# Kernel optimization log

Hardware: AMD Instinct MI355X
Metric: run time of the kernel (lower is better)

Reference implementation:

```python
import jax, jax.numpy as jnp
import numpy as np

KK = 27  # 3x3x3 kernel taps


def conv3d(x, w, b):
    # plain 3D conv, stride 1, pad 1 (the offset-prediction conv)
    y = jax.lax.conv_general_dilated(
        x, w, window_strides=(1, 1, 1),
        padding=((1, 1), (1, 1), (1, 1)),
        dimension_numbers=('NCDHW', 'OIDHW', 'NCDHW'))
    return y + b[None, :, None, None, None]


def deform_conv3d_hw(x, offset, weight):
    # DCN with 3x3x3 kernel, offsets only along H,W (dimension='HW');
    # temporal tap positions are integers so trilinear -> bilinear in HW.
    N, C, T, H, W = x.shape
    off = offset.reshape(N, KK, 2, T, H, W)  # interleaved (h_off, w_off) per tap
    kk = jnp.arange(KK)
    kt = kk // 9 - 1
    kh = (kk // 3) % 3 - 1
    kw = kk % 3 - 1
    t_idx = jnp.arange(T)[None, :, None, None] + kt[:, None, None, None]  # (KK,T,1,1)
    t_ok = jnp.broadcast_to((t_idx >= 0) & (t_idx < T), (KK, T, H, W))
    t_cb = jnp.broadcast_to(jnp.clip(t_idx, 0, T - 1), (KK, T, H, W))
    ph = (jnp.arange(H)[None, None, :, None] + kh[:, None, None, None]).astype(x.dtype)[None] + off[:, :, 0]
    pw = (jnp.arange(W)[None, None, None, :] + kw[:, None, None, None]).astype(x.dtype)[None] + off[:, :, 1]
    h0f = jnp.floor(ph); w0f = jnp.floor(pw)
    lh = (ph - h0f)[:, None]  # (N,1,KK,T,H,W)
    lw = (pw - w0f)[:, None]
    h0 = h0f.astype(jnp.int32); w0 = w0f.astype(jnp.int32)
    h1 = h0 + 1; w1 = w0 + 1

    def gather(hi, wi):
        ok = t_ok[None] & (hi >= 0) & (hi < H) & (wi >= 0) & (wi < W)
        hic = jnp.clip(hi, 0, H - 1)
        wic = jnp.clip(wi, 0, W - 1)
        def g1(xb, okb, hb, wb):
            # xb: (C,T,H,W); index arrays: (KK,T,H,W) -> (C,KK,T,H,W)
            return jnp.where(okb[None], xb[:, t_cb, hb, wb], 0.0)
        return jax.vmap(g1)(x, ok, hic, wic)  # (N,C,KK,T,H,W)

    acc = gather(h0, w0) * ((1 - lh) * (1 - lw))
    acc = acc + gather(h0, w1) * ((1 - lh) * lw)
    acc = acc + gather(h1, w0) * (lh * (1 - lw))
    acc = acc + gather(h1, w1) * (lh * lw)
    Cout = weight.shape[0]
    return jnp.einsum('nckthw,ock->nothw', acc, weight.reshape(Cout, C, KK))


def setup_inputs() -> dict:
    key = jax.random.key(0)
    ks = jax.random.split(key, 7)
    N, C, T, H, W = 1, 64, 7, 64, 64
    x = jax.random.normal(ks[0], (N, C, T, H, W), jnp.float32)
    sc_off = 0.01  # keep predicted offsets small (original zero-inits them)
    sc_w = 1.0 / np.sqrt(C * KK)
    w_off0 = jax.random.normal(ks[1], (2 * KK, C, 3, 3, 3), jnp.float32) * sc_off
    b_off0 = jax.random.normal(ks[2], (2 * KK,), jnp.float32) * sc_off
    w0 = jax.random.normal(ks[3], (C, C, 3, 3, 3), jnp.float32) * sc_w
    w_off1 = jax.random.normal(ks[4], (2 * KK, C, 3, 3, 3), jnp.float32) * sc_off
    b_off1 = jax.random.normal(ks[5], (2 * KK,), jnp.float32) * sc_off
    w1 = jax.random.normal(ks[6], (C, C, 3, 3, 3), jnp.float32) * sc_w
    return {"x": x, "w_off0": w_off0, "b_off0": b_off0, "w0": w0,
            "w_off1": w_off1, "b_off1": b_off1, "w1": w1}


def reference(x, w_off0, b_off0, w0, w_off1, b_off1, w1):
    y = deform_conv3d_hw(x, conv3d(x, w_off0, b_off0), w0)
    y = jax.nn.leaky_relu(y, negative_slope=0.1)
    y = deform_conv3d_hw(y, conv3d(y, w_off1, b_off1), w1)
    return y + x
```

## Files before the change

### kernel.cpp

```cpp
#include <hip/hip_runtime.h>

#define T_ 7
#define H_ 64
#define W_ 64
#define KK_ 27
#define HW_ 4096
#define THW_ 28672
#define CO_OFF 54
#define OFFSTR 56

using frag_ab = __attribute__((ext_vector_type(8))) short;
using f32x4   = __attribute__((ext_vector_type(4))) float;

__device__ __forceinline__ unsigned short f2bf(float v) {
    unsigned u = __float_as_uint(v);
    unsigned r = u + 0x7FFFu + ((u >> 16) & 1u);
    return (unsigned short)(r >> 16);
}
__device__ __forceinline__ float bf2f(unsigned short h) {
    return __uint_as_float(((unsigned)h) << 16);
}
__device__ __forceinline__ void split_bf(float v, unsigned short& hi, unsigned short& lo) {
    hi = f2bf(v);
    lo = f2bf(v - bf2f(hi));
}
__device__ __forceinline__ void split_tr(float v, unsigned short& hi, unsigned short& lo) {
    unsigned u = __float_as_uint(v);
    hi = (unsigned short)(u >> 16);
    float r = v - __uint_as_float(u & 0xFFFF0000u);
    lo = (unsigned short)(__float_as_uint(r) >> 16);
}

__global__ void prep_wt_kernel(const float* __restrict__ w_off0,
                               const float* __restrict__ w_off1,
                               const float* __restrict__ w0,
                               const float* __restrict__ w1,
                               unsigned short* __restrict__ wc0,
                               unsigned short* __restrict__ wc1,
                               unsigned short* __restrict__ wd0,
                               unsigned short* __restrict__ wd1) {
    int idx = blockIdx.x * 256 + threadIdx.x;
    int which = idx / 110592;
    int r = idx - which * 110592;
    int tap = r >> 12;
    int o = (r >> 6) & 63;
    int c = r & 63;
    const float* src;
    unsigned short* dst;
    int Co;
    switch (which) {
        case 0:  src = w_off0; dst = wc0; Co = CO_OFF; break;
        case 1:  src = w_off1; dst = wc1; Co = CO_OFF; break;
        case 2:  src = w0;     dst = wd0; Co = 64;     break;
        default: src = w1;     dst = wd1; Co = 64;     break;
    }
    float v = 0.f;
    if (o < Co) v = src[o * 1728 + c * 27 + tap];
    unsigned short hi, lo;
    split_bf(v, hi, lo);
    dst[tap * 8192 + 0 * 4096 + o * 64 + c] = hi;
    dst[tap * 8192 + 1 * 4096 + o * 64 + c] = lo;
}

__global__ void __launch_bounds__(256) transpose_kernel(
    const float* __restrict__ x, float* __restrict__ xT) {
    __shared__ float lx[64][65];
    const int tid = threadIdx.x;
    const int base = blockIdx.x * 64;
    const int w = tid & 63, cg = tid >> 6;
#pragma unroll
    for (int i = 0; i < 16; ++i) {
        const int c = cg * 16 + i;
        lx[c][w] = x[c * THW_ + base + w];
    }
    __syncthreads();
    const int c = tid & 63, j0 = tid >> 6;
#pragma unroll
    for (int j = 0; j < 16; ++j) {
        const int wp = j * 4 + j0;
        xT[(base + wp) * 64 + c] = lx[c][wp];
    }
}


__global__ void __launch_bounds__(512, 8) conv_off_kernel(
    const float* __restrict__ xT, const unsigned short* __restrict__ wB,
    const float* __restrict__ bias, float* __restrict__ offT) {
    __shared__ __align__(16) unsigned short A_l[2][32][64];
    __shared__ __align__(16) unsigned short B_l[2][64][64];
    const int tid = threadIdx.x;
    const int bid = blockIdx.x;
    const int t = bid >> 7, h = (bid >> 1) & 63, wh = bid & 1;
    const int wg = wh * 32;
    const int c4 = tid & 15;
    const int wp = tid >> 4;
    const int lane = tid & 63, wid = tid >> 6;
    const int wtile = wid & 1, otile = wid >> 1;
    const int ln15 = lane & 15, kg = lane >> 4;
    const int arow = wtile * 16 + ln15;
    const int brow = otile * 16 + ln15;
    const int posb = t * HW_ + h * W_ + wg;
    const int bo = (tid >> 3) & 63, bc8 = tid & 7;
    const int bi = (bc8 * 8) ^ ((bo & 7) << 3);

    f32x4 acc = {0.f, 0.f, 0.f, 0.f};

    for (int k = 0; k < KK_; ++k) {
        const int kt = k / 9 - 1, kh = (k / 3) % 3 - 1, kw = k % 3 - 1;
        const int ts = t + kt, hs = h + kh, wsr = wg + wp + kw;
        const bool ok = ((unsigned)ts < 7u) & ((unsigned)hs < 64u) & ((unsigned)wsr < 64u);
        float4 v = make_float4(0.f, 0.f, 0.f, 0.f);
        if (ok)
            v = *reinterpret_cast<const float4*>(xT + (ts * HW_ + hs * W_ + wsr) * 64 + c4 * 4);
        ushort4 hv, lv;
        split_tr(v.x, hv.x, lv.x); split_tr(v.y, hv.y, lv.y);
        split_tr(v.z, hv.z, lv.z); split_tr(v.w, hv.w, lv.w);
        const int ci = (c4 * 4) ^ ((wp & 7) << 3);
        *reinterpret_cast<ushort4*>(&A_l[0][wp][ci]) = hv;
        *reinterpret_cast<ushort4*>(&A_l[1][wp][ci]) = lv;
        const unsigned short* wt = wB + k * 8192 + bo * 64 + bc8 * 8;
        *reinterpret_cast<frag_ab*>(&B_l[0][bo][bi]) =
            *reinterpret_cast<const frag_ab*>(wt);
        *reinterpret_cast<frag_ab*>(&B_l[1][bo][bi]) =
            *reinterpret_cast<const frag_ab*>(wt + 4096);
        __syncthreads();
#pragma unroll
        for (int ks = 0; ks < 2; ++ks) {
            const int ka = ks * 32 + kg * 8;
            const frag_ab ah = *reinterpret_cast<const frag_ab*>(&A_l[0][arow][ka ^ ((arow & 7) << 3)]);
            const frag_ab al = *reinterpret_cast<const frag_ab*>(&A_l[1][arow][ka ^ ((arow & 7) << 3)]);
            const frag_ab bh = *reinterpret_cast<const frag_ab*>(&B_l[0][brow][ka ^ ((brow & 7) << 3)]);
            const frag_ab bl = *reinterpret_cast<const frag_ab*>(&B_l[1][brow][ka ^ ((brow & 7) << 3)]);
            acc = __builtin_amdgcn_mfma_f32_16x16x32_bf16(ah, bh, acc, 0, 0, 0);
            acc = __builtin_amdgcn_mfma_f32_16x16x32_bf16(ah, bl, acc, 0, 0, 0);
            acc = __builtin_amdgcn_mfma_f32_16x16x32_bf16(al, bh, acc, 0, 0, 0);
        }
        __syncthreads();
    }

    const int o = otile * 16 + ln15;
    if (o < CO_OFF) {
        const float b = bias[o];
#pragma unroll
        for (int reg = 0; reg < 4; ++reg) {
            const int wl_ = wtile * 16 + kg * 4 + reg;
            offT[(posb + wl_) * OFFSTR + o] = acc[reg] + b;
        }
    }
}

template <int MODE>
__global__ void __launch_bounds__(512, 8) dcn_kernel(
    const float* __restrict__ xT, const float* __restrict__ offT,
    const unsigned short* __restrict__ wB, const float* __restrict__ resid,
    float* __restrict__ out) {
    __shared__ __align__(16) unsigned short A_l[2][32][64];
    __shared__ __align__(16) unsigned short B_l[2][64][64];
    __shared__ float ep[32][65];
    const int tid = threadIdx.x;
    const int bid = blockIdx.x;
    const int t = bid >> 7, h = (bid >> 1) & 63, wh = bid & 1;
    const int wg = wh * 32;
    const int c4 = tid & 15;
    const int wp = tid >> 4;
    const int lane = tid & 63, wid = tid >> 6;
    const int wtile = wid & 1, otile = wid >> 1;
    const int ln15 = lane & 15, kg = lane >> 4;
    const int arow = wtile * 16 + ln15;
    const int brow = otile * 16 + ln15;
    const int posb = t * HW_ + h * W_ + wg;
    const int bo = (tid >> 3) & 63, bc8 = tid & 7;
    const int bi = (bc8 * 8) ^ ((bo & 7) << 3);

    f32x4 acc = {0.f, 0.f, 0.f, 0.f};
    const int w = wg + wp;
    const float* offp = offT + (posb + wp) * OFFSTR;

    for (int k = 0; k < KK_; ++k) {
        const int kt = k / 9 - 1, kh = (k / 3) % 3 - 1, kw = k % 3 - 1;
        const int ts = t + kt;
        const bool tok = (unsigned)ts < 7u;
        const int tcb = ts < 0 ? 0 : (ts > 6 ? 6 : ts);
        const float2 of2 = *reinterpret_cast<const float2*>(offp + 2 * k);
        const float ph = (float)(h + kh) + of2.x;
        const float pw = (float)(w + kw) + of2.y;
        const float h0f = floorf(ph), w0f = floorf(pw);
        const float fh = ph - h0f, fw = pw - w0f;
        const int h0 = (int)h0f, w0i = (int)w0f;
        const int h1 = h0 + 1, w1i = w0i + 1;
        const bool h0k = (unsigned)h0 < 64u, h1k = (unsigned)h1 < 64u;
        const bool w0k = (unsigned)w0i < 64u, w1k = (unsigned)w1i < 64u;
        const int tb = tcb * HW_;
        const int h0c = (h0 < 0 ? 0 : (h0 > 63 ? 63 : h0)) * W_;
        const int h1c = (h1 < 0 ? 0 : (h1 > 63 ? 63 : h1)) * W_;
        const int w0c = w0i < 0 ? 0 : (w0i > 63 ? 63 : w0i);
        const int w1c = w1i < 0 ? 0 : (w1i > 63 ? 63 : w1i);
        const float f0 = (tok && h0k && w0k) ? (1.f - fh) * (1.f - fw) : 0.f;
        const float f1 = (tok && h0k && w1k) ? (1.f - fh) * fw : 0.f;
        const float f2 = (tok && h1k && w0k) ? fh * (1.f - fw) : 0.f;
        const float f3 = (tok && h1k && w1k) ? fh * fw : 0.f;
        const int cb = c4 * 4;
        const float4 A = *reinterpret_cast<const float4*>(xT + (tb + h0c + w0c) * 64 + cb);
        const float4 B = *reinterpret_cast<const float4*>(xT + (tb + h0c + w1c) * 64 + cb);
        const float4 C = *reinterpret_cast<const float4*>(xT + (tb + h1c + w0c) * 64 + cb);
        const float4 D = *reinterpret_cast<const float4*>(xT + (tb + h1c + w1c) * 64 + cb);
        float s0 = fmaf(f0, A.x, fmaf(f1, B.x, fmaf(f2, C.x, f3 * D.x)));
        float s1 = fmaf(f0, A.y, fmaf(f1, B.y, fmaf(f2, C.y, f3 * D.y)));
        float s2 = fmaf(f0, A.z, fmaf(f1, B.z, fmaf(f2, C.z, f3 * D.z)));
        float s3 = fmaf(f0, A.w, fmaf(f1, B.w, fmaf(f2, C.w, f3 * D.w)));
        ushort4 hv, lv;
        split_tr(s0, hv.x, lv.x); split_tr(s1, hv.y, lv.y);
        split_tr(s2, hv.z, lv.z); split_tr(s3, hv.w, lv.w);
        const int ci = (cb) ^ ((wp & 7) << 3);
        *reinterpret_cast<ushort4*>(&A_l[0][wp][ci]) = hv;
        *reinterpret_cast<ushort4*>(&A_l[1][wp][ci]) = lv;
        const unsigned short* wt = wB + k * 8192 + bo * 64 + bc8 * 8;
        *reinterpret_cast<frag_ab*>(&B_l[0][bo][bi]) =
            *reinterpret_cast<const frag_ab*>(wt);
        *reinterpret_cast<frag_ab*>(&B_l[1][bo][bi]) =
            *reinterpret_cast<const frag_ab*>(wt + 4096);
        __syncthreads();
#pragma unroll
        for (int ks = 0; ks < 2; ++ks) {
            const int ka = ks * 32 + kg * 8;
            const frag_ab ah = *reinterpret_cast<const frag_ab*>(&A_l[0][arow][ka ^ ((arow & 7) << 3)]);
            const frag_ab al = *reinterpret_cast<const frag_ab*>(&A_l[1][arow][ka ^ ((arow & 7) << 3)]);
            const frag_ab bh = *reinterpret_cast<const frag_ab*>(&B_l[0][brow][ka ^ ((brow & 7) << 3)]);
            const frag_ab bl = *reinterpret_cast<const frag_ab*>(&B_l[1][brow][ka ^ ((brow & 7) << 3)]);
            acc = __builtin_amdgcn_mfma_f32_16x16x32_bf16(ah, bh, acc, 0, 0, 0);
            acc = __builtin_amdgcn_mfma_f32_16x16x32_bf16(ah, bl, acc, 0, 0, 0);
            acc = __builtin_amdgcn_mfma_f32_16x16x32_bf16(al, bh, acc, 0, 0, 0);
        }
        __syncthreads();
    }

    const int o = otile * 16 + ln15;
    if (MODE == 0) {
#pragma unroll
        for (int reg = 0; reg < 4; ++reg) {
            const int wl_ = wtile * 16 + kg * 4 + reg;
            float v = acc[reg];
            v = v > 0.f ? v : 0.1f * v;
            out[(posb + wl_) * 64 + o] = v;
        }
    } else {
#pragma unroll
        for (int reg = 0; reg < 4; ++reg) {
            const int wl_ = wtile * 16 + kg * 4 + reg;
            ep[wl_][o] = acc[reg];
        }
        __syncthreads();
        const int w2 = tid & 31, og = tid >> 5;
#pragma unroll
        for (int i = 0; i < 4; ++i) {
            const int oc = og + i * 16;
            out[oc * THW_ + posb + w2] = ep[w2][oc] + resid[oc * THW_ + posb + w2];
        }
    }
}

extern "C" void kernel_launch(void* const* d_in, const int* in_sizes, int n_in,
                              void* d_out, int out_size, void* d_ws, size_t ws_size,
                              hipStream_t stream) {
    (void)in_sizes; (void)n_in; (void)out_size; (void)ws_size;
    const float* x      = (const float*)d_in[0];
    const float* w_off0 = (const float*)d_in[1];
    const float* b_off0 = (const float*)d_in[2];
    const float* w0     = (const float*)d_in[3];
    const float* w_off1 = (const float*)d_in[4];
    const float* b_off1 = (const float*)d_in[5];
    const float* w1     = (const float*)d_in[6];
    float* out = (float*)d_out;

    float* ws = (float*)d_ws;
    float* xT   = ws;
    float* yT   = xT + 64 * THW_;
    float* offT = yT + 64 * THW_;
    unsigned short* wc0 = (unsigned short*)(offT + THW_ * OFFSTR);
    unsigned short* wc1 = wc0 + 221184;
    unsigned short* wd0 = wc1 + 221184;
    unsigned short* wd1 = wd0 + 221184;

    prep_wt_kernel<<<1728, 256, 0, stream>>>(w_off0, w_off1, w0, w1,
                                             wc0, wc1, wd0, wd1);
    transpose_kernel<<<448, 256, 0, stream>>>(x, xT);
    conv_off_kernel<<<896, 512, 0, stream>>>(xT, wc0, b_off0, offT);
    dcn_kernel<0><<<896, 512, 0, stream>>>(xT, offT, wd0, nullptr, yT);
    conv_off_kernel<<<896, 512, 0, stream>>>(yT, wc1, b_off1, offT);
    dcn_kernel<1><<<896, 512, 0, stream>>>(yT, offT, wd1, x, out);
}
```

Baseline: 265.4 us.

## Prefetch next tap's inputs and weights into registers during MFMA

Both the offset conv kernel and the deformable conv kernel now issue the global loads for the next kernel tap (input samples, bilinear corners, offsets, weights) into registers before running the current tap's MFMAs. The results are written to shared memory after a barrier, so global memory latency is meant to overlap with matrix compute. The cost is higher register pressure, which could reduce occupancy under launch_bounds(512,8). Each iteration also now has two barriers.

```diff
diff --git a/kernel.cpp b/kernel.cpp
--- a/kernel.cpp
+++ b/kernel.cpp
@@ -102,12 +102,12 @@
     const int posb = t * HW_ + h * W_ + wg;
     const int bo = (tid >> 3) & 63, bc8 = tid & 7;
     const int bi = (bc8 * 8) ^ ((bo & 7) << 3);
+    const int ci = (c4 * 4) ^ ((wp & 7) << 3);
 
     f32x4 acc = {0.f, 0.f, 0.f, 0.f};
 
-    for (int k = 0; k < KK_; ++k) {
-        const int kt = k / 9 - 1, kh = (k / 3) % 3 - 1, kw = k % 3 - 1;
-        const int ts = t + kt, hs = h + kh, wsr = wg + wp + kw;
+    {
+        const int ts = t - 1, hs = h - 1, wsr = wg + wp - 1;
         const bool ok = ((unsigned)ts < 7u) & ((unsigned)hs < 64u) & ((unsigned)wsr < 64u);
         float4 v = make_float4(0.f, 0.f, 0.f, 0.f);
         if (ok)
@@ -115,15 +115,29 @@
         ushort4 hv, lv;
         split_tr(v.x, hv.x, lv.x); split_tr(v.y, hv.y, lv.y);
         split_tr(v.z, hv.z, lv.z); split_tr(v.w, hv.w, lv.w);
-        const int ci = (c4 * 4) ^ ((wp & 7) << 3);
         *reinterpret_cast<ushort4*>(&A_l[0][wp][ci]) = hv;
         *reinterpret_cast<ushort4*>(&A_l[1][wp][ci]) = lv;
-        const unsigned short* wt = wB + k * 8192 + bo * 64 + bc8 * 8;
-        *reinterpret_cast<frag_ab*>(&B_l[0][bo][bi]) =
-            *reinterpret_cast<const frag_ab*>(wt);
-        *reinterpret_cast<frag_ab*>(&B_l[1][bo][bi]) =
-            *reinterpret_cast<const frag_ab*>(wt + 4096);
-        __syncthreads();
+        const unsigned short* wt = wB + bo * 64 + bc8 * 8;
+        *reinterpret_cast<frag_ab*>(&B_l[0][bo][bi]) = *reinterpret_cast<const frag_ab*>(wt);
+        *reinterpret_cast<frag_ab*>(&B_l[1][bo][bi]) = *reinterpret_cast<const frag_ab*>(wt + 4096);
+    }
+    __syncthreads();
+
+    float4 vn;
+    frag_ab b0n, b1n;
+    for (int k = 0; k < KK_; ++k) {
+        if (k + 1 < KK_) {
+            const int kk = k + 1;
+            const int kt = kk / 9 - 1, kh = (kk / 3) % 3 - 1, kw = kk % 3 - 1;
+            const int ts = t + kt, hs = h + kh, wsr = wg + wp + kw;
+            const bool ok = ((unsigned)ts < 7u) & ((unsigned)hs < 64u) & ((unsigned)wsr < 64u);
+            vn = make_float4(0.f, 0.f, 0.f, 0.f);
+            if (ok)
+                vn = *reinterpret_cast<const float4*>(xT + (ts * HW_ + hs * W_ + wsr) * 64 + c4 * 4);
+            const unsigned short* wt = wB + kk * 8192 + bo * 64 + bc8 * 8;
+            b0n = *reinterpret_cast<const frag_ab*>(wt);
+            b1n = *reinterpret_cast<const frag_ab*>(wt + 4096);
+        }
 #pragma unroll
         for (int ks = 0; ks < 2; ++ks) {
             const int ka = ks * 32 + kg * 8;
@@ -134,6 +148,16 @@
             acc = __builtin_amdgcn_mfma_f32_16x16x32_bf16(ah, bh, acc, 0, 0, 0);
             acc = __builtin_amdgcn_mfma_f32_16x16x32_bf16(ah, bl, acc, 0, 0, 0);
             acc = __builtin_amdgcn_mfma_f32_16x16x32_bf16(al, bh, acc, 0, 0, 0);
+        }
+        __syncthreads();
+        if (k + 1 < KK_) {
+            ushort4 hv, lv;
+            split_tr(vn.x, hv.x, lv.x); split_tr(vn.y, hv.y, lv.y);
+            split_tr(vn.z, hv.z, lv.z); split_tr(vn.w, hv.w, lv.w);
+            *reinterpret_cast<ushort4*>(&A_l[0][wp][ci]) = hv;
+            *reinterpret_cast<ushort4*>(&A_l[1][wp][ci]) = lv;
+            *reinterpret_cast<frag_ab*>(&B_l[0][bo][bi]) = b0n;
+            *reinterpret_cast<frag_ab*>(&B_l[1][bo][bi]) = b1n;
         }
         __syncthreads();
     }
@@ -171,17 +195,19 @@
     const int posb = t * HW_ + h * W_ + wg;
     const int bo = (tid >> 3) & 63, bc8 = tid & 7;
     const int bi = (bc8 * 8) ^ ((bo & 7) << 3);
+    const int ci = (c4 * 4) ^ ((wp & 7) << 3);
+    const int cb = c4 * 4;
 
     f32x4 acc = {0.f, 0.f, 0.f, 0.f};
     const int w = wg + wp;
     const float* offp = offT + (posb + wp) * OFFSTR;
 
-    for (int k = 0; k < KK_; ++k) {
-        const int kt = k / 9 - 1, kh = (k / 3) % 3 - 1, kw = k % 3 - 1;
+    auto corners = [&](int kk, float2 of2, int& i0, int& i1, int& i2, int& i3,
+                       float& f0, float& f1, float& f2, float& f3) {
+        const int kt = kk / 9 - 1, kh = (kk / 3) % 3 - 1, kw = kk % 3 - 1;
         const int ts = t + kt;
         const bool tok = (unsigned)ts < 7u;
         const int tcb = ts < 0 ? 0 : (ts > 6 ? 6 : ts);
-        const float2 of2 = *reinterpret_cast<const float2*>(offp + 2 * k);
         const float ph = (float)(h + kh) + of2.x;
         const float pw = (float)(w + kw) + of2.y;
         const float h0f = floorf(ph), w0f = floorf(pw);
@@ -195,15 +221,24 @@
         const int h1c = (h1 < 0 ? 0 : (h1 > 63 ? 63 : h1)) * W_;
         const int w0c = w0i < 0 ? 0 : (w0i > 63 ? 63 : w0i);
         const int w1c = w1i < 0 ? 0 : (w1i > 63 ? 63 : w1i);
-        const float f0 = (tok && h0k && w0k) ? (1.f - fh) * (1.f - fw) : 0.f;
-        const float f1 = (tok && h0k && w1k) ? (1.f - fh) * fw : 0.f;
-        const float f2 = (tok && h1k && w0k) ? fh * (1.f - fw) : 0.f;
-        const float f3 = (tok && h1k && w1k) ? fh * fw : 0.f;
-        const int cb = c4 * 4;
-        const float4 A = *reinterpret_cast<const float4*>(xT + (tb + h0c + w0c) * 64 + cb);
-        const float4 B = *reinterpret_cast<const float4*>(xT + (tb + h0c + w1c) * 64 + cb);
-        const float4 C = *reinterpret_cast<const float4*>(xT + (tb + h1c + w0c) * 64 + cb);
-        const float4 D = *reinterpret_cast<const float4*>(xT + (tb + h1c + w1c) * 64 + cb);
+        i0 = tb + h0c + w0c; i1 = tb + h0c + w1c;
+        i2 = tb + h1c + w0c; i3 = tb + h1c + w1c;
+        f0 = (tok && h0k && w0k) ? (1.f - fh) * (1.f - fw) : 0.f;
+        f1 = (tok && h0k && w1k) ? (1.f - fh) * fw : 0.f;
+        f2 = (tok && h1k && w0k) ? fh * (1.f - fw) : 0.f;
+        f3 = (tok && h1k && w1k) ? fh * fw : 0.f;
+    };
+
+    float2 ofN;
+    {
+        const float2 of0 = *reinterpret_cast<const float2*>(offp);
+        ofN = *reinterpret_cast<const float2*>(offp + 2);
+        int i0, i1, i2, i3; float f0, f1, f2, f3;
+        corners(0, of0, i0, i1, i2, i3, f0, f1, f2, f3);
+        const float4 A = *reinterpret_cast<const float4*>(xT + i0 * 64 + cb);
+        const float4 B = *reinterpret_cast<const float4*>(xT + i1 * 64 + cb);
+        const float4 C = *reinterpret_cast<const float4*>(xT + i2 * 64 + cb);
+        const float4 D = *reinterpret_cast<const float4*>(xT + i3 * 64 + cb);
         float s0 = fmaf(f0, A.x, fmaf(f1, B.x, fmaf(f2, C.x, f3 * D.x)));
         float s1 = fmaf(f0, A.y, fmaf(f1, B.y, fmaf(f2, C.y, f3 * D.y)));
         float s2 = fmaf(f0, A.z, fmaf(f1, B.z, fmaf(f2, C.z, f3 * D.z)));
@@ -211,15 +246,31 @@
         ushort4 hv, lv;
         split_tr(s0, hv.x, lv.x); split_tr(s1, hv.y, lv.y);
         split_tr(s2, hv.z, lv.z); split_tr(s3, hv.w, lv.w);
-        const int ci = (cb) ^ ((wp & 7) << 3);
         *reinterpret_cast<ushort4*>(&A_l[0][wp][ci]) = hv;
         *reinterpret_cast<ushort4*>(&A_l[1][wp][ci]) = lv;
-        const unsigned short* wt = wB + k * 8192 + bo * 64 + bc8 * 8;
-        *reinterpret_cast<frag_ab*>(&B_l[0][bo][bi]) =
-            *reinterpret_cast<const frag_ab*>(wt);
-        *reinterpret_cast<frag_ab*>(&B_l[1][bo][bi]) =
-            *reinterpret_cast<const frag_ab*>(wt + 4096);
-        __syncthreads();
+        const unsigned short* wt = wB + bo * 64 + bc8 * 8;
+        *reinterpret_cast<frag_ab*>(&B_l[0][bo][bi]) = *reinterpret_cast<const frag_ab*>(wt);
+        *reinterpret_cast<frag_ab*>(&B_l[1][bo][bi]) = *reinterpret_cast<const frag_ab*>(wt + 4096);
+    }
+    __syncthreads();
+
+    float4 An, Bn, Cn, Dn;
+    float f0n, f1n, f2n, f3n;
+    frag_ab b0n, b1n;
+    for (int k = 0; k < KK_; ++k) {
+        if (k + 1 < KK_) {
+            int i0, i1, i2, i3;
+            corners(k + 1, ofN, i0, i1, i2, i3, f0n, f1n, f2n, f3n);
+            An = *reinterpret_cast<const float4*>(xT + i0 * 64 + cb);
+            Bn = *reinterpret_cast<const float4*>(xT + i1 * 64 + cb);
+            Cn = *reinterpret_cast<const float4*>(xT + i2 * 64 + cb);
+            Dn = *reinterpret_cast<const float4*>(xT + i3 * 64 + cb);
+            const unsigned short* wt = wB + (k + 1) * 8192 + bo * 64 + bc8 * 8;
+            b0n = *reinterpret_cast<const frag_ab*>(wt);
+            b1n = *reinterpret_cast<const frag_ab*>(wt + 4096);
+            if (k + 2 < KK_)
+                ofN = *reinterpret_cast<const float2*>(offp + 2 * (k + 2));
+        }
 #pragma unroll
         for (int ks = 0; ks < 2; ++ks) {
             const int ka = ks * 32 + kg * 8;
@@ -230,6 +281,20 @@
             acc = __builtin_amdgcn_mfma_f32_16x16x32_bf16(ah, bh, acc, 0, 0, 0);
             acc = __builtin_amdgcn_mfma_f32_16x16x32_bf16(ah, bl, acc, 0, 0, 0);
             acc = __builtin_amdgcn_mfma_f32_16x16x32_bf16(al, bh, acc, 0, 0, 0);
+        }
+        __syncthreads();
+        if (k + 1 < KK_) {
+            float s0 = fmaf(f0n, An.x, fmaf(f1n, Bn.x, fmaf(f2n, Cn.x, f3n * Dn.x)));
+            float s1 = fmaf(f0n, An.y, fmaf(f1n, Bn.y, fmaf(f2n, Cn.y, f3n * Dn.y)));
+            float s2 = fmaf(f0n, An.z, fmaf(f1n, Bn.z, fmaf(f2n, Cn.z, f3n * Dn.z)));
+            float s3 = fmaf(f0n, An.w, fmaf(f1n, Bn.w, fmaf(f2n, Cn.w, f3n * Dn.w)));
+            ushort4 hv, lv;
+            split_tr(s0, hv.x, lv.x); split_tr(s1, hv.y, lv.y);
+            split_tr(s2, hv.z, lv.z); split_tr(s3, hv.w, lv.w);
+            *reinterpret_cast<ushort4*>(&A_l[0][wp][ci]) = hv;
+            *reinterpret_cast<ushort4*>(&A_l[1][wp][ci]) = lv;
+            *reinterpret_cast<frag_ab*>(&B_l[0][bo][bi]) = b0n;
+            *reinterpret_cast<frag_ab*>(&B_l[1][bo][bi]) = b1n;
         }
         __syncthreads();
     }
```

Result: no change. 260.7 us (-1.8%).
